# Optimization experiments

Measured on AMD Instinct MI355X. Metric: run time of the kernel, lower is better.

## Reference

```python
import math
import jax, jax.numpy as jnp
import numpy as np

B, T, D = 4, 4096, 512


def setup_inputs() -> dict:
    key = jax.random.key(0)
    k1, _ = jax.random.split(key)
    x = jax.random.normal(k1, (B, T, D), dtype=jnp.float32)
    log_alpha = jnp.zeros((), dtype=jnp.float32)
    return {"x": x, "log_alpha": log_alpha}


def _gelu_tanh(x):
    c = math.sqrt(2.0 / math.pi)
    return 0.5 * x * (1.0 + jnp.tanh(c * (x + 0.044715 * x * x * x)))


def reference(x, log_alpha):
    Bx, Tx, Dx = x.shape
    alpha = jax.nn.softplus(log_alpha)
    # F.normalize(dim=-1): x / max(||x||, eps)
    norm = jnp.maximum(jnp.linalg.norm(x, axis=-1, keepdims=True), 1e-12)
    x_norm = x / norm
    sim = jnp.einsum("btd,bsd->bts", x_norm, x_norm)  # [B,T,T]
    # causal mask: triu incl. diagonal (col >= row) filled with -2.0
    row = jnp.arange(Tx)[:, None]
    col = jnp.arange(Tx)[None, :]
    mask = col >= row  # [T,T]
    sim = jnp.where(mask[None], jnp.float32(-2.0), sim)
    max_sim = jnp.max(sim, axis=-1)  # [B,T]
    max_sim = jnp.maximum(max_sim, -1.0)
    familiarity = (max_sim + 1.0) * 0.5
    novelty = 1.0 - familiarity
    gate = 1.0 + alpha * novelty[..., None]  # [B,T,1]
    return _gelu_tanh(x * gate)
```

## Files before the change

### kernel.cpp

```cpp
#include <hip/hip_runtime.h>
#include <hip/hip_bf16.h>
#include <math.h>

#define B_ 4
#define T_ 4096
#define D_ 512
#define BT 128
#define BK 32
#define NT (T_ / BT)
#define NPAIR (NT * (NT + 1) / 2)


typedef short bf16x8 __attribute__((ext_vector_type(8)));
typedef float f32x4 __attribute__((ext_vector_type(4)));

__device__ __forceinline__ unsigned short f2bf(float f) {
    unsigned u = __float_as_uint(f);
    u += 0x7FFFu + ((u >> 16) & 1u);
    return (unsigned short)(u >> 16);
}
__device__ __forceinline__ unsigned f2ord(float f) {
    unsigned u = __float_as_uint(f);
    return (u & 0x80000000u) ? ~u : (u | 0x80000000u);
}
__device__ __forceinline__ float ord2f(unsigned u) {
    unsigned b = (u & 0x80000000u) ? (u ^ 0x80000000u) : ~u;
    return __uint_as_float(b);
}

__device__ __forceinline__ void async16(const unsigned short* g, unsigned short* l) {
    __builtin_amdgcn_global_load_lds(
        (const __attribute__((address_space(1))) unsigned int*)g,
        (__attribute__((address_space(3))) unsigned int*)l, 16, 0, 0);
}

__global__ __launch_bounds__(256) void k_norm(const float* __restrict__ x,
                                              unsigned short* __restrict__ xn,
                                              unsigned* __restrict__ maxsim) {
    int w = (blockIdx.x * 256 + threadIdx.x) >> 6;
    int lane = threadIdx.x & 63;
    const float4* xr = (const float4*)(x + (size_t)w * D_);
    float4 a = xr[lane];
    float4 b = xr[lane + 64];
    float ss = a.x * a.x + a.y * a.y + a.z * a.z + a.w * a.w +
               b.x * b.x + b.y * b.y + b.z * b.z + b.w * b.w;
#pragma unroll
    for (int off = 32; off > 0; off >>= 1) ss += __shfl_xor(ss, off);
    float inv = 1.0f / fmaxf(sqrtf(ss), 1e-12f);
    unsigned u0 = (unsigned)f2bf(a.x * inv) | ((unsigned)f2bf(a.y * inv) << 16);
    unsigned u1 = (unsigned)f2bf(a.z * inv) | ((unsigned)f2bf(a.w * inv) << 16);
    unsigned u2 = (unsigned)f2bf(b.x * inv) | ((unsigned)f2bf(b.y * inv) << 16);
    unsigned u3 = (unsigned)f2bf(b.z * inv) | ((unsigned)f2bf(b.w * inv) << 16);
    uint2* xo = (uint2*)(xn + (size_t)w * D_);
    xo[lane]      = make_uint2(u0, u1);
    xo[lane + 64] = make_uint2(u2, u3);
    if (lane == 0) maxsim[w] = f2ord(-2.0f);
}

__global__ __launch_bounds__(256, 4) void k_maxsim(const unsigned short* __restrict__ xn,
                                                   unsigned* __restrict__ maxsim) {
    __shared__ __align__(16) unsigned short As[BT * BK];
    __shared__ __align__(16) unsigned short Bs[BT * BK];
    const int b = blockIdx.y;
    const int p = blockIdx.x;
    int ti = (int)((sqrtf(8.0f * (float)p + 1.0f) - 1.0f) * 0.5f);
    while ((ti + 1) * (ti + 2) / 2 <= p) ti++;
    while (ti * (ti + 1) / 2 > p) ti--;
    const int si = p - ti * (ti + 1) / 2;
    const int t0 = ti * BT, s0 = si * BT;

    const int tid = threadIdx.x;
    const int wave = tid >> 6, lane = tid & 63;
    const int wm = wave >> 1, wn = wave & 1;
    const int qa = lane >> 4, la = lane & 15;
    const int swz = (la >> 1) & 3;

    const unsigned short* Ab = xn + (size_t)(b * T_ + t0) * D_;
    const unsigned short* Bb = xn + (size_t)(b * T_ + s0) * D_;

    f32x4 acc[4][4];
#pragma unroll
    for (int i = 0; i < 4; i++)
#pragma unroll
        for (int j = 0; j < 4; j++) acc[i][j] = (f32x4){0.f, 0.f, 0.f, 0.f};

    for (int k0 = 0; k0 < D_; k0 += BK) {
#pragma unroll
        for (int j = 0; j < 2; j++) {
            int c = j * 256 + tid;
            int row = c >> 2;
            int chunk = (c & 3) ^ ((row >> 1) & 3);
            int ldsbase = (j * 256 + wave * 64) * 8;
            async16(Ab + (size_t)row * D_ + k0 + chunk * 8, &As[ldsbase]);
            async16(Bb + (size_t)row * D_ + k0 + chunk * 8, &Bs[ldsbase]);
        }
        __syncthreads();
        bf16x8 af[4], bfr[4];
#pragma unroll
        for (int i = 0; i < 4; i++)
            af[i] = *(const bf16x8*)&As[(wm * 64 + i * 16 + la) * BK + (qa ^ swz) * 8];
#pragma unroll
        for (int j = 0; j < 4; j++)
            bfr[j] = *(const bf16x8*)&Bs[(wn * 64 + j * 16 + la) * BK + (qa ^ swz) * 8];
#pragma unroll
        for (int i = 0; i < 4; i++)
#pragma unroll
            for (int j = 0; j < 4; j++)
                acc[i][j] = __builtin_amdgcn_mfma_f32_16x16x32_bf16(af[i], bfr[j], acc[i][j], 0, 0, 0);
        __syncthreads();
    }

    const bool diag = (ti == si);
#pragma unroll
    for (int i = 0; i < 4; i++) {
#pragma unroll
        for (int r = 0; r < 4; r++) {
            int tl = wm * 64 + i * 16 + qa * 4 + r;
            float m = -2.0f;
#pragma unroll
            for (int j = 0; j < 4; j++) {
                int sl = wn * 64 + j * 16 + la;
                float v = acc[i][j][r];
                if (!diag || sl < tl) m = fmaxf(m, v);
            }
#pragma unroll
            for (int off = 1; off < 16; off <<= 1) m = fmaxf(m, __shfl_xor(m, off));
            if (la == 0) atomicMax(&maxsim[b * T_ + t0 + tl], f2ord(m));
        }
    }
}

__device__ __forceinline__ float gelu_tanh(float y) {
    float t = tanhf(0.7978845608028654f * (y + 0.044715f * y * y * y));
    return 0.5f * y * (1.0f + t);
}

__global__ __launch_bounds__(256) void k_gate(const float* __restrict__ x,
                                              const float* __restrict__ log_alpha,
                                              const unsigned* __restrict__ maxsim,
                                              float* __restrict__ out) {
    int idx = blockIdx.x * 256 + threadIdx.x;
    float la = log_alpha[0];
    float alpha = (la > 20.0f) ? la : log1pf(expf(la));
    int row = idx >> 7;
    float m = fmaxf(ord2f(maxsim[row]), -1.0f);
    float novelty = 1.0f - (m + 1.0f) * 0.5f;
    float gate = 1.0f + alpha * novelty;
    float4 v = ((const float4*)x)[idx];
    float4 o;
    o.x = gelu_tanh(v.x * gate);
    o.y = gelu_tanh(v.y * gate);
    o.z = gelu_tanh(v.z * gate);
    o.w = gelu_tanh(v.w * gate);
    ((float4*)out)[idx] = o;
}

extern "C" void kernel_launch(void* const* d_in, const int* in_sizes, int n_in,
                              void* d_out, int out_size, void* d_ws, size_t ws_size,
                              hipStream_t stream) {
    const float* x = (const float*)d_in[0];
    const float* log_alpha = (const float*)d_in[1];
    float* out = (float*)d_out;

    unsigned* maxsim = (unsigned*)d_ws;
    unsigned short* xn = (unsigned short*)((char*)d_ws + 65536);

    const int rows = B_ * T_;
    k_norm<<<rows / 4, 256, 0, stream>>>(x, xn, maxsim);

    dim3 g2(NPAIR, B_);
    k_maxsim<<<g2, 256, 0, stream>>>(xn, maxsim);

    k_gate<<<(B_ * T_ * D_ / 4) / 256, 256, 0, stream>>>(x, log_alpha, maxsim, out);
}
```

Before: 158.8 us.

## Double-buffer LDS tiles with register-staged prefetch in maxsim GEMM

```diff
diff --git a/kernel.cpp b/kernel.cpp
--- a/kernel.cpp
+++ b/kernel.cpp
@@ -7,6 +7,7 @@
 #define D_ 512
 #define BT 128
 #define BK 32
+#define STEPS (D_ / BK)
 #define NT (T_ / BT)
 #define NPAIR (NT * (NT + 1) / 2)
 
@@ -28,10 +29,9 @@
     return __uint_as_float(b);
 }
 
-__device__ __forceinline__ void async16(const unsigned short* g, unsigned short* l) {
-    __builtin_amdgcn_global_load_lds(
-        (const __attribute__((address_space(1))) unsigned int*)g,
-        (__attribute__((address_space(3))) unsigned int*)l, 16, 0, 0);
+__device__ __forceinline__ void barrier_lgkm_only() {
+    __builtin_amdgcn_s_waitcnt(0xC07F);
+    __builtin_amdgcn_s_barrier();
 }
 
 __global__ __launch_bounds__(256) void k_norm(const float* __restrict__ x,
@@ -57,10 +57,9 @@
     if (lane == 0) maxsim[w] = f2ord(-2.0f);
 }
 
-__global__ __launch_bounds__(256, 4) void k_maxsim(const unsigned short* __restrict__ xn,
-                                                   unsigned* __restrict__ maxsim) {
-    __shared__ __align__(16) unsigned short As[BT * BK];
-    __shared__ __align__(16) unsigned short Bs[BT * BK];
+__global__ __launch_bounds__(256) void k_maxsim(const unsigned short* __restrict__ xn,
+                                                unsigned* __restrict__ maxsim) {
+    __shared__ __align__(16) unsigned short Buf[2][256 * BK];
     const int b = blockIdx.y;
     const int p = blockIdx.x;
     int ti = (int)((sqrtf(8.0f * (float)p + 1.0f) - 1.0f) * 0.5f);
@@ -78,36 +77,71 @@
     const unsigned short* Ab = xn + (size_t)(b * T_ + t0) * D_;
     const unsigned short* Bb = xn + (size_t)(b * T_ + s0) * D_;
 
+    const int srow = tid >> 2;
+    const int sq = tid & 3;
+    const unsigned short* gA0 = Ab + (size_t)srow * D_ + sq * 8;
+    const unsigned short* gA1 = gA0 + (size_t)64 * D_;
+    const unsigned short* gB0 = Bb + (size_t)srow * D_ + sq * 8;
+    const unsigned short* gB1 = gB0 + (size_t)64 * D_;
+    const int wpos = (sq ^ ((srow >> 1) & 3)) * 8;
+    const int wo0 = (srow) * BK + wpos;
+    const int wo1 = (srow + 64) * BK + wpos;
+    const int wo2 = (srow + 128) * BK + wpos;
+    const int wo3 = (srow + 192) * BK + wpos;
+
     f32x4 acc[4][4];
 #pragma unroll
     for (int i = 0; i < 4; i++)
 #pragma unroll
         for (int j = 0; j < 4; j++) acc[i][j] = (f32x4){0.f, 0.f, 0.f, 0.f};
 
-    for (int k0 = 0; k0 < D_; k0 += BK) {
-#pragma unroll
-        for (int j = 0; j < 2; j++) {
-            int c = j * 256 + tid;
-            int row = c >> 2;
-            int chunk = (c & 3) ^ ((row >> 1) & 3);
-            int ldsbase = (j * 256 + wave * 64) * 8;
-            async16(Ab + (size_t)row * D_ + k0 + chunk * 8, &As[ldsbase]);
-            async16(Bb + (size_t)row * D_ + k0 + chunk * 8, &Bs[ldsbase]);
-        }
-        __syncthreads();
+    uint4 r0 = *(const uint4*)(gA0);
+    uint4 r1 = *(const uint4*)(gA1);
+    uint4 r2 = *(const uint4*)(gB0);
+    uint4 r3 = *(const uint4*)(gB1);
+    {
+        unsigned short* b0 = &Buf[0][0];
+        *(uint4*)&b0[wo0] = r0;
+        *(uint4*)&b0[wo1] = r1;
+        *(uint4*)&b0[wo2] = r2;
+        *(uint4*)&b0[wo3] = r3;
+    }
+    r0 = *(const uint4*)(gA0 + BK);
+    r1 = *(const uint4*)(gA1 + BK);
+    r2 = *(const uint4*)(gB0 + BK);
+    r3 = *(const uint4*)(gB1 + BK);
+
+#pragma unroll 2
+    for (int k = 0; k < STEPS; ++k) {
+        unsigned short* cur = &Buf[k & 1][0];
+        unsigned short* nxt = &Buf[(k + 1) & 1][0];
+        barrier_lgkm_only();
+
+        const int ko = (k + 2 < STEPS ? k + 2 : STEPS - 1) * BK;
+        uint4 n0 = *(const uint4*)(gA0 + ko);
+        uint4 n1 = *(const uint4*)(gA1 + ko);
+        uint4 n2 = *(const uint4*)(gB0 + ko);
+        uint4 n3 = *(const uint4*)(gB1 + ko);
+
         bf16x8 af[4], bfr[4];
 #pragma unroll
         for (int i = 0; i < 4; i++)
-            af[i] = *(const bf16x8*)&As[(wm * 64 + i * 16 + la) * BK + (qa ^ swz) * 8];
+            af[i] = *(const bf16x8*)&cur[(wm * 64 + i * 16 + la) * BK + (qa ^ swz) * 8];
 #pragma unroll
         for (int j = 0; j < 4; j++)
-            bfr[j] = *(const bf16x8*)&Bs[(wn * 64 + j * 16 + la) * BK + (qa ^ swz) * 8];
+            bfr[j] = *(const bf16x8*)&cur[(128 + wn * 64 + j * 16 + la) * BK + (qa ^ swz) * 8];
+
+        *(uint4*)&nxt[wo0] = r0;
+        *(uint4*)&nxt[wo1] = r1;
+        *(uint4*)&nxt[wo2] = r2;
+        *(uint4*)&nxt[wo3] = r3;
+        r0 = n0; r1 = n1; r2 = n2; r3 = n3;
+
 #pragma unroll
         for (int i = 0; i < 4; i++)
 #pragma unroll
             for (int j = 0; j < 4; j++)
                 acc[i][j] = __builtin_amdgcn_mfma_f32_16x16x32_bf16(af[i], bfr[j], acc[i][j], 0, 0, 0);
-        __syncthreads();
     }
 
     const bool diag = (ti == si);
```

Result: slower. 165.7 us (+4.3%).

## Load MFMA operands directly from global into registers with double buffering

Applied to the files above, without the earlier changes.

```diff
diff --git a/kernel.cpp b/kernel.cpp
--- a/kernel.cpp
+++ b/kernel.cpp
@@ -6,7 +6,6 @@
 #define T_ 4096
 #define D_ 512
 #define BT 128
-#define BK 32
 #define NT (T_ / BT)
 #define NPAIR (NT * (NT + 1) / 2)
 
@@ -26,12 +25,6 @@
 __device__ __forceinline__ float ord2f(unsigned u) {
     unsigned b = (u & 0x80000000u) ? (u ^ 0x80000000u) : ~u;
     return __uint_as_float(b);
-}
-
-__device__ __forceinline__ void async16(const unsigned short* g, unsigned short* l) {
-    __builtin_amdgcn_global_load_lds(
-        (const __attribute__((address_space(1))) unsigned int*)g,
-        (__attribute__((address_space(3))) unsigned int*)l, 16, 0, 0);
 }
 
 __global__ __launch_bounds__(256) void k_norm(const float* __restrict__ x,
@@ -57,10 +50,8 @@
     if (lane == 0) maxsim[w] = f2ord(-2.0f);
 }
 
-__global__ __launch_bounds__(256, 4) void k_maxsim(const unsigned short* __restrict__ xn,
-                                                   unsigned* __restrict__ maxsim) {
-    __shared__ __align__(16) unsigned short As[BT * BK];
-    __shared__ __align__(16) unsigned short Bs[BT * BK];
+__global__ __launch_bounds__(256) void k_maxsim(const unsigned short* __restrict__ xn,
+                                                unsigned* __restrict__ maxsim) {
     const int b = blockIdx.y;
     const int p = blockIdx.x;
     int ti = (int)((sqrtf(8.0f * (float)p + 1.0f) - 1.0f) * 0.5f);
@@ -73,10 +64,9 @@
     const int wave = tid >> 6, lane = tid & 63;
     const int wm = wave >> 1, wn = wave & 1;
     const int qa = lane >> 4, la = lane & 15;
-    const int swz = (la >> 1) & 3;
 
-    const unsigned short* Ab = xn + (size_t)(b * T_ + t0) * D_;
-    const unsigned short* Bb = xn + (size_t)(b * T_ + s0) * D_;
+    const unsigned short* pa = xn + (size_t)(b * T_ + t0 + wm * 64 + la) * D_ + qa * 8;
+    const unsigned short* pb = xn + (size_t)(b * T_ + s0 + wn * 64 + la) * D_ + qa * 8;
 
     f32x4 acc[4][4];
 #pragma unroll
@@ -84,30 +74,29 @@
 #pragma unroll
         for (int j = 0; j < 4; j++) acc[i][j] = (f32x4){0.f, 0.f, 0.f, 0.f};
 
-    for (int k0 = 0; k0 < D_; k0 += BK) {
+    bf16x8 sa[2][4], sb[2][4];
 #pragma unroll
-        for (int j = 0; j < 2; j++) {
-            int c = j * 256 + tid;
-            int row = c >> 2;
-            int chunk = (c & 3) ^ ((row >> 1) & 3);
-            int ldsbase = (j * 256 + wave * 64) * 8;
-            async16(Ab + (size_t)row * D_ + k0 + chunk * 8, &As[ldsbase]);
-            async16(Bb + (size_t)row * D_ + k0 + chunk * 8, &Bs[ldsbase]);
+    for (int i = 0; i < 4; i++) sa[0][i] = *(const bf16x8*)(pa + (size_t)i * 16 * D_);
+#pragma unroll
+    for (int j = 0; j < 4; j++) sb[0][j] = *(const bf16x8*)(pb + (size_t)j * 16 * D_);
+
+#pragma unroll 2
+    for (int k = 0; k < 16; ++k) {
+        const int cur = k & 1, nxt = cur ^ 1;
+        if (k < 15) {
+            const int ko = (k + 1) * 32;
+#pragma unroll
+            for (int i = 0; i < 4; i++)
+                sa[nxt][i] = *(const bf16x8*)(pa + (size_t)i * 16 * D_ + ko);
+#pragma unroll
+            for (int j = 0; j < 4; j++)
+                sb[nxt][j] = *(const bf16x8*)(pb + (size_t)j * 16 * D_ + ko);
         }
-        __syncthreads();
-        bf16x8 af[4], bfr[4];
-#pragma unroll
-        for (int i = 0; i < 4; i++)
-            af[i] = *(const bf16x8*)&As[(wm * 64 + i * 16 + la) * BK + (qa ^ swz) * 8];
-#pragma unroll
-        for (int j = 0; j < 4; j++)
-            bfr[j] = *(const bf16x8*)&Bs[(wn * 64 + j * 16 + la) * BK + (qa ^ swz) * 8];
 #pragma unroll
         for (int i = 0; i < 4; i++)
 #pragma unroll
             for (int j = 0; j < 4; j++)
-                acc[i][j] = __builtin_amdgcn_mfma_f32_16x16x32_bf16(af[i], bfr[j], acc[i][j], 0, 0, 0);
-        __syncthreads();
+                acc[i][j] = __builtin_amdgcn_mfma_f32_16x16x32_bf16(sa[cur][i], sb[cur][j], acc[i][j], 0, 0, 0);
     }
 
     const bool diag = (ti == si);
```

Result: slower. 229.5 us (+44.5%).

## Triple-buffer LDS tiles with async prefetch two steps ahead in maxsim GEMM

Applied to the files above, without the earlier changes.

```diff
diff --git a/kernel.cpp b/kernel.cpp
--- a/kernel.cpp
+++ b/kernel.cpp
@@ -7,6 +7,7 @@
 #define D_ 512
 #define BT 128
 #define BK 32
+#define STEPS (D_ / BK)
 #define NT (T_ / BT)
 #define NPAIR (NT * (NT + 1) / 2)
 
@@ -57,10 +58,9 @@
     if (lane == 0) maxsim[w] = f2ord(-2.0f);
 }
 
-__global__ __launch_bounds__(256, 4) void k_maxsim(const unsigned short* __restrict__ xn,
-                                                   unsigned* __restrict__ maxsim) {
-    __shared__ __align__(16) unsigned short As[BT * BK];
-    __shared__ __align__(16) unsigned short Bs[BT * BK];
+__global__ __launch_bounds__(256) void k_maxsim(const unsigned short* __restrict__ xn,
+                                                unsigned* __restrict__ maxsim) {
+    __shared__ __align__(16) unsigned short Buf[3][8192];
     const int b = blockIdx.y;
     const int p = blockIdx.x;
     int ti = (int)((sqrtf(8.0f * (float)p + 1.0f) - 1.0f) * 0.5f);
@@ -78,23 +78,43 @@
     const unsigned short* Ab = xn + (size_t)(b * T_ + t0) * D_;
     const unsigned short* Bb = xn + (size_t)(b * T_ + s0) * D_;
 
+    const int c0 = tid,        r0_ = c0 >> 2, g0 = (c0 & 3) ^ ((r0_ >> 1) & 3);
+    const int c1 = 256 + tid,  r1_ = c1 >> 2, g1 = (c1 & 3) ^ ((r1_ >> 1) & 3);
+    const unsigned short* gA0 = Ab + (size_t)r0_ * D_ + g0 * 8;
+    const unsigned short* gA1 = Ab + (size_t)r1_ * D_ + g1 * 8;
+    const unsigned short* gB0 = Bb + (size_t)r0_ * D_ + g0 * 8;
+    const unsigned short* gB1 = Bb + (size_t)r1_ * D_ + g1 * 8;
+    const int ldsb0 = (wave * 64) * 8;
+    const int ldsb1 = (256 + wave * 64) * 8;
+
+#define STAGE(step, st)                                            \
+    do {                                                           \
+        async16(gA0 + (step) * BK, &Buf[st][ldsb0]);               \
+        async16(gB0 + (step) * BK, &Buf[st][4096 + ldsb0]);        \
+        async16(gA1 + (step) * BK, &Buf[st][ldsb1]);               \
+        async16(gB1 + (step) * BK, &Buf[st][4096 + ldsb1]);        \
+    } while (0)
+
     f32x4 acc[4][4];
 #pragma unroll
     for (int i = 0; i < 4; i++)
 #pragma unroll
         for (int j = 0; j < 4; j++) acc[i][j] = (f32x4){0.f, 0.f, 0.f, 0.f};
 
-    for (int k0 = 0; k0 < D_; k0 += BK) {
+    STAGE(0, 0);
+    STAGE(1, 1);
+
 #pragma unroll
-        for (int j = 0; j < 2; j++) {
-            int c = j * 256 + tid;
-            int row = c >> 2;
-            int chunk = (c & 3) ^ ((row >> 1) & 3);
-            int ldsbase = (j * 256 + wave * 64) * 8;
-            async16(Ab + (size_t)row * D_ + k0 + chunk * 8, &As[ldsbase]);
-            async16(Bb + (size_t)row * D_ + k0 + chunk * 8, &Bs[ldsbase]);
-        }
-        __syncthreads();
+    for (int k = 0; k < STEPS; ++k) {
+        const int cur = k % 3;
+        if (k == STEPS - 1) __builtin_amdgcn_s_waitcnt(0x0F70);
+        else                __builtin_amdgcn_s_waitcnt(0x0F74);
+        __builtin_amdgcn_s_barrier();
+        __asm__ __volatile__("" ::: "memory");
+        if (k + 2 < STEPS) STAGE(k + 2, (k + 2) % 3);
+
+        const unsigned short* As = &Buf[cur][0];
+        const unsigned short* Bs = &Buf[cur][4096];
         bf16x8 af[4], bfr[4];
 #pragma unroll
         for (int i = 0; i < 4; i++)
@@ -107,8 +127,8 @@
 #pragma unroll
             for (int j = 0; j < 4; j++)
                 acc[i][j] = __builtin_amdgcn_mfma_f32_16x16x32_bf16(af[i], bfr[j], acc[i][j], 0, 0, 0);
-        __syncthreads();
     }
+#undef STAGE
 
     const bool diag = (ti == si);
 #pragma unroll
```

New measurement: 144.2 us. 9.2% less time.
